# Kernel optimization log

Measured on AMD Instinct MI355X. Metric: run time of the kernel, lower is better.

The kernel has to match this reference:

```python
import jax, jax.numpy as jnp
import numpy as np

N = 100000   # total nodes in batched graph
E = 320000   # total edges
B = 128      # number of graphs in batch
D_IN = 128
H = 256
OUT = 10
L = 4        # num_layers - 1 conv layers
EPS = 1e-6


def setup_inputs() -> dict:
    key = jax.random.key(0)
    ks = jax.random.split(key, 8)
    h = jax.random.normal(ks[0], (N, D_IN), dtype=jnp.float32)
    src = jax.random.randint(ks[1], (E,), 0, N)
    dst = jax.random.randint(ks[2], (E,), 0, N)
    batch_ids = jnp.sort(jax.random.randint(ks[3], (N,), 0, B))
    s = 0.05
    W_first = jax.random.normal(ks[4], (D_IN, H), dtype=jnp.float32) * s
    b_first = jnp.zeros((H,), jnp.float32)
    W_rest = jax.random.normal(ks[5], (L - 1, H, H), dtype=jnp.float32) * s
    b_rest = jnp.zeros((L - 1, H), jnp.float32)
    gamma = jnp.ones((L, H), jnp.float32)
    beta = jnp.zeros((L, H), jnp.float32)
    mean_scale = jnp.ones((L, H), jnp.float32)
    W_pred = jax.random.normal(ks[6], (H, OUT), dtype=jnp.float32) * s
    b_pred = jnp.zeros((OUT,), jnp.float32)
    return dict(h=h, src=src, dst=dst, batch_ids=batch_ids,
                W_first=W_first, b_first=b_first, W_rest=W_rest, b_rest=b_rest,
                gamma=gamma, beta=beta, mean_scale=mean_scale,
                W_pred=W_pred, b_pred=b_pred)


def _graph_conv(h, W, b, src, dst, dinv_src, dinv_dst):
    # DGL GraphConv, norm='both': D_dst^{-1/2} A D_src^{-1/2} h W + b
    x = h * dinv_src[:, None]
    m = jax.ops.segment_sum(x[src], dst, num_segments=N)
    m = m * dinv_dst[:, None]
    return m @ W + b


def _graph_norm(h, gamma, beta, ms, batch_ids, counts):
    # GraphNorm: per-graph mean (scaled by learnable mean_scale) and std
    mean = jax.ops.segment_sum(h, batch_ids, num_segments=B) / counts[:, None]
    sub = h - mean[batch_ids] * ms
    var = jax.ops.segment_sum(sub * sub, batch_ids, num_segments=B) / counts[:, None]
    inv_std = jax.lax.rsqrt(var + EPS)
    return gamma * sub * inv_std[batch_ids] + beta


def reference(h, src, dst, batch_ids, W_first, b_first, W_rest, b_rest,
              gamma, beta, mean_scale, W_pred, b_pred):
    ones_e = jnp.ones((E,), h.dtype)
    deg_out = jnp.maximum(jax.ops.segment_sum(ones_e, src, num_segments=N), 1.0)
    deg_in = jnp.maximum(jax.ops.segment_sum(ones_e, dst, num_segments=N), 1.0)
    dinv_src = jax.lax.rsqrt(deg_out)
    dinv_dst = jax.lax.rsqrt(deg_in)
    counts = jnp.maximum(
        jax.ops.segment_sum(jnp.ones((N,), h.dtype), batch_ids, num_segments=B), 1.0)

    for i in range(L):
        x = h
        if i == 0:
            h = _graph_conv(h, W_first, b_first, src, dst, dinv_src, dinv_dst)
        else:
            h = _graph_conv(h, W_rest[i - 1], b_rest[i - 1], src, dst, dinv_src, dinv_dst)
        h = _graph_norm(h, gamma[i], beta[i], mean_scale[i], batch_ids, counts)
        if i != 0:
            h = jax.nn.relu(h) + x
        else:
            h = jax.nn.relu(h)

    pooled = jax.ops.segment_sum(h, batch_ids, num_segments=B)  # [B, H]
    # dropout is identity at eval
    return pooled @ W_pred + b_pred
```

## Files before the change

kernel.cpp:

```cpp
#include <hip/hip_runtime.h>

#define N_NODES 100000
#define N_PAD   100096
#define N_EDGES 320000
#define NB      128
#define DIN     128
#define H       256
#define OUT_DIM 10
#define EPSV    1e-6f
#define SCAN_B  256
#define PSLICES 32

typedef unsigned short bf16_t;
typedef __attribute__((ext_vector_type(8))) short bf16x8;
typedef __attribute__((ext_vector_type(4))) float f32x4;

__device__ __forceinline__ float bf2f(bf16_t u) {
    union { unsigned int i; float f; } x;
    x.i = ((unsigned int)u) << 16;
    return x.f;
}
__device__ __forceinline__ bf16_t f2bf(float f) {
    union { float f; unsigned int i; } x;
    x.f = f;
    unsigned int r = x.i + 0x7fffu + ((x.i >> 16) & 1u);
    return (bf16_t)(r >> 16);
}

__global__ void k_edge_deg(const int* __restrict__ src, const int* __restrict__ dst,
                           int* deg_out, int* deg_in) {
    int e = blockIdx.x * blockDim.x + threadIdx.x;
    if (e < N_EDGES) {
        atomicAdd(&deg_out[src[e]], 1);
        atomicAdd(&deg_in[dst[e]], 1);
    }
}

__global__ void k_dinv(const int* __restrict__ deg_out, const int* __restrict__ deg_in,
                       float* dinv_src, float* dinv_dst) {
    int n = blockIdx.x * blockDim.x + threadIdx.x;
    if (n < N_NODES) {
        dinv_src[n] = rsqrtf((float)max(deg_out[n], 1));
        dinv_dst[n] = rsqrtf((float)max(deg_in[n], 1));
    }
}

__global__ void k_gstart(const int* __restrict__ bid, int* __restrict__ gstart,
                         float* __restrict__ countsf) {
    int b = threadIdx.x;
    if (b <= NB) {
        int lo = 0, hi = N_NODES;
        while (lo < hi) {
            int mid = (lo + hi) >> 1;
            if (bid[mid] < b) lo = mid + 1; else hi = mid;
        }
        gstart[b] = lo;
    }
    __syncthreads();
    if (b < NB) countsf[b] = (float)max(gstart[b + 1] - gstart[b], 1);
}

__global__ void k_scan1(const int* __restrict__ deg, int* incl, int* bsums) {
    __shared__ int s[SCAN_B];
    int i = blockIdx.x * SCAN_B + threadIdx.x;
    int v = (i < N_NODES) ? deg[i] : 0;
    s[threadIdx.x] = v;
    __syncthreads();
    for (int d = 1; d < SCAN_B; d <<= 1) {
        int t = (threadIdx.x >= d) ? s[threadIdx.x - d] : 0;
        __syncthreads();
        s[threadIdx.x] += t;
        __syncthreads();
    }
    if (i < N_NODES) incl[i] = s[threadIdx.x];
    if (threadIdx.x == SCAN_B - 1) bsums[blockIdx.x] = s[threadIdx.x];
}

__global__ void k_scan2(const int* __restrict__ bsums, int* boffs, int nb) {
    __shared__ int s[512];
    int t = threadIdx.x;
    int v = (t < nb) ? bsums[t] : 0;
    s[t] = v;
    __syncthreads();
    for (int d = 1; d < 512; d <<= 1) {
        int x = (t >= d) ? s[t - d] : 0;
        __syncthreads();
        s[t] += x;
        __syncthreads();
    }
    if (t < nb) boffs[t] = s[t] - v;
}

__global__ void k_scan3(const int* __restrict__ deg, const int* __restrict__ incl,
                        const int* __restrict__ boffs, int* row_start, int* cursor) {
    int i = blockIdx.x * blockDim.x + threadIdx.x;
    if (i < N_NODES) {
        int ex = incl[i] - deg[i] + boffs[i / SCAN_B];
        row_start[i] = ex;
        cursor[i]    = ex;
    }
    if (i == 0) row_start[N_NODES] = N_EDGES;
}

__global__ void k_scatter(const int* __restrict__ src, const int* __restrict__ dst,
                          int* cursor, int* csr_src) {
    int e = blockIdx.x * blockDim.x + threadIdx.x;
    if (e < N_EDGES) {
        int slot = atomicAdd(&cursor[dst[e]], 1);
        csr_src[slot] = src[e];
    }
}

__global__ void k_wt_first(const float* __restrict__ W, bf16_t* __restrict__ Wt) {
    int idx = blockIdx.x * 256 + threadIdx.x;
    if (idx >= H * DIN) return;
    int c = idx / DIN, k = idx % DIN;
    Wt[idx] = f2bf(W[k * H + c]);
}
__global__ void k_wt_rest(const float* __restrict__ W, bf16_t* __restrict__ Wt) {
    int idx = blockIdx.x * 256 + threadIdx.x;
    if (idx >= 3 * H * H) return;
    int l = idx / (H * H);
    int rem = idx % (H * H);
    int c = rem / H, k = rem % H;
    Wt[idx] = f2bf(W[(size_t)l * H * H + k * H + c]);
}

__global__ void k_prescale(const float* __restrict__ h, const float* __restrict__ dinv_s,
                           bf16_t* __restrict__ hs) {
    int idx = blockIdx.x * blockDim.x + threadIdx.x;
    if (idx >= N_NODES * (DIN / 4)) return;
    int n = idx >> 5;
    float w = dinv_s[n];
    float4 v = reinterpret_cast<const float4*>(h)[idx];
    ushort4 o;
    o.x = f2bf(v.x * w); o.y = f2bf(v.y * w);
    o.z = f2bf(v.z * w); o.w = f2bf(v.w * w);
    reinterpret_cast<ushort4*>(hs)[idx] = o;
}

template <int NC, bool PS>
__global__ void k_agg(const bf16_t* __restrict__ hx, const float* __restrict__ dinv_s,
                      const float* __restrict__ dinv_d, const int* __restrict__ row_start,
                      const int* __restrict__ csr_src, bf16_t* __restrict__ m) {
    constexpr int VEC = NC / 64;
    int gid  = blockIdx.x * blockDim.x + threadIdx.x;
    int v    = gid >> 6;
    int lane = gid & 63;
    if (v >= N_NODES) return;
    float acc[VEC] = {};
    int s0 = row_start[v], s1 = row_start[v + 1];

    auto body = [&](int ei) {
        int si = csr_src[ei];
        float wv = 1.f;
        if constexpr (!PS) wv = dinv_s[si];
        if constexpr (VEC == 4) {
            ushort4 r = *reinterpret_cast<const ushort4*>(hx + (size_t)si * NC + lane * 4);
            acc[0] += bf2f(r.x) * wv; acc[1] += bf2f(r.y) * wv;
            acc[2] += bf2f(r.z) * wv; acc[3] += bf2f(r.w) * wv;
        } else {
            ushort2 r = *reinterpret_cast<const ushort2*>(hx + (size_t)si * NC + lane * 2);
            acc[0] += bf2f(r.x) * wv; acc[1] += bf2f(r.y) * wv;
        }
    };

    int e = s0;
    for (; e + 3 < s1; e += 4) { body(e); body(e + 1); body(e + 2); body(e + 3); }
    for (; e < s1; ++e) body(e);

    float wd = dinv_d[v];
    if constexpr (VEC == 4) {
        ushort4 o;
        o.x = f2bf(acc[0] * wd); o.y = f2bf(acc[1] * wd);
        o.z = f2bf(acc[2] * wd); o.w = f2bf(acc[3] * wd);
        *reinterpret_cast<ushort4*>(m + (size_t)v * NC + lane * 4) = o;
    } else {
        ushort2 o; o.x = f2bf(acc[0] * wd); o.y = f2bf(acc[1] * wd);
        *reinterpret_cast<ushort2*>(m + (size_t)v * NC + lane * 2) = o;
    }
}

template <int K>
__global__ __launch_bounds__(256) void k_gemm_mfma(const bf16_t* __restrict__ A,
                                                   const bf16_t* __restrict__ Wt,
                                                   const float* __restrict__ bias,
                                                   const int* __restrict__ bid,
                                                   bf16_t* __restrict__ C,
                                                   float* __restrict__ gsum,
                                                   float* __restrict__ gsumsq) {
    __shared__ bf16_t cT[64][H + 8];
    __shared__ int bid_lds[64];

    const int tid  = threadIdx.x;
    const int wave = tid >> 6;
    const int lane = tid & 63;
    const int row0 = blockIdx.x * 64;
    const int col0 = wave * 64;
    const int lr = lane & 15;
    const int lg = lane >> 4;

    if (tid < 64) {
        int r = row0 + tid;
        bid_lds[tid] = (r < N_NODES) ? bid[r] : -1;
    }

    const bf16_t* Ar = A  + (size_t)(row0 + lr) * K + lg * 8;
    const bf16_t* Br = Wt + (size_t)(col0 + lr) * K + lg * 8;

    f32x4 acc[4][4] = {};

    #pragma unroll
    for (int ks = 0; ks < K / 32; ++ks) {
        bf16x8 a[4], b[4];
        #pragma unroll
        for (int mt = 0; mt < 4; ++mt)
            a[mt] = *reinterpret_cast<const bf16x8*>(Ar + (size_t)mt * 16 * K + ks * 32);
        #pragma unroll
        for (int nt = 0; nt < 4; ++nt)
            b[nt] = *reinterpret_cast<const bf16x8*>(Br + (size_t)nt * 16 * K + ks * 32);
        #pragma unroll
        for (int mt = 0; mt < 4; ++mt)
            #pragma unroll
            for (int nt = 0; nt < 4; ++nt)
                acc[mt][nt] = __builtin_amdgcn_mfma_f32_16x16x32_bf16(a[mt], b[nt], acc[mt][nt], 0, 0, 0);
    }

    #pragma unroll
    for (int nt = 0; nt < 4; ++nt) {
        int c = col0 + nt * 16 + lr;
        float bs = bias[c];
        #pragma unroll
        for (int mt = 0; mt < 4; ++mt) {
            #pragma unroll
            for (int j = 0; j < 4; ++j)
                cT[mt * 16 + lg * 4 + j][c] = f2bf(acc[mt][nt][j] + bs);
        }
    }
    __syncthreads();

    #pragma unroll
    for (int it = 0; it < 8; ++it) {
        int i = it * 256 + tid;
        int r = i >> 5;
        int s = i & 31;
        *reinterpret_cast<uint4*>(C + (size_t)(row0 + r) * H + s * 8) =
            *reinterpret_cast<const uint4*>(&cT[r][s * 8]);
    }

    {
        const int c = tid;
        float s = 0.f, q = 0.f;
        int gprev = bid_lds[0];
        #pragma unroll 8
        for (int r = 0; r < 64; ++r) {
            int g = bid_lds[r];
            if (g < 0) break;
            if (g != gprev) {
                atomicAdd(&gsum[gprev * H + c], s);
                atomicAdd(&gsumsq[gprev * H + c], q);
                s = 0.f; q = 0.f; gprev = g;
            }
            float v = bf2f(cT[r][c]);
            s += v; q += v * v;
        }
        if (gprev >= 0) {
            atomicAdd(&gsum[gprev * H + c], s);
            atomicAdd(&gsumsq[gprev * H + c], q);
        }
    }
}

template <bool RES>
__global__ void k_norm(const bf16_t* __restrict__ y, const bf16_t* __restrict__ resid,
                       const int* __restrict__ bid, const float* __restrict__ gsum,
                       const float* __restrict__ gsumsq, const float* __restrict__ countsf,
                       const float* __restrict__ gamma, const float* __restrict__ beta,
                       const float* __restrict__ msc, bf16_t* __restrict__ outp) {
    int idx = blockIdx.x * blockDim.x + threadIdx.x;
    if (idx >= N_NODES * (H / 4)) return;
    int n  = idx >> 6;
    int f4 = idx & 63;
    int b  = bid[n];
    float rc = 1.0f / countsf[b];
    float4 s4  = reinterpret_cast<const float4*>(gsum)[b * 64 + f4];
    float4 q4  = reinterpret_cast<const float4*>(gsumsq)[b * 64 + f4];
    float4 g4  = reinterpret_cast<const float4*>(gamma)[f4];
    float4 be4 = reinterpret_cast<const float4*>(beta)[f4];
    float4 m4  = reinterpret_cast<const float4*>(msc)[f4];
    ushort4 yv = reinterpret_cast<const ushort4*>(y)[idx];

    auto nrm = [&](float s, float q, float ga, float be, float m, float yy) {
        float mean = s * rc, ex2 = q * rc;
        float mm   = mean * m;
        float var  = ex2 - 2.f * mean * mm + mm * mm;
        float a    = ga * rsqrtf(var + EPSV);
        return fmaxf(yy * a + (be - a * mm), 0.f);
    };
    float o0 = nrm(s4.x, q4.x, g4.x, be4.x, m4.x, bf2f(yv.x));
    float o1 = nrm(s4.y, q4.y, g4.y, be4.y, m4.y, bf2f(yv.y));
    float o2 = nrm(s4.z, q4.z, g4.z, be4.z, m4.z, bf2f(yv.z));
    float o3 = nrm(s4.w, q4.w, g4.w, be4.w, m4.w, bf2f(yv.w));
    if constexpr (RES) {
        ushort4 r = reinterpret_cast<const ushort4*>(resid)[idx];
        o0 += bf2f(r.x); o1 += bf2f(r.y); o2 += bf2f(r.z); o3 += bf2f(r.w);
    }
    ushort4 o;
    o.x = f2bf(o0); o.y = f2bf(o1); o.z = f2bf(o2); o.w = f2bf(o3);
    reinterpret_cast<ushort4*>(outp)[idx] = o;
}

__global__ void k_pool(const bf16_t* __restrict__ hf, const int* __restrict__ gstart,
                       float* pooled) {
    int b = blockIdx.x, sl = blockIdx.y, f = threadIdx.x;
    int n0 = gstart[b], n1 = gstart[b + 1];
    int cnt = n1 - n0;
    int lo = n0 + (int)((long long)cnt * sl / PSLICES);
    int hi = n0 + (int)((long long)cnt * (sl + 1) / PSLICES);
    if (lo >= hi) return;
    float s = 0.f;
    for (int n = lo; n < hi; ++n) s += bf2f(hf[(size_t)n * H + f]);
    atomicAdd(&pooled[b * H + f], s);
}

__global__ void k_pred(const float* __restrict__ pooled, const float* __restrict__ Wp,
                       const float* __restrict__ bp, float* __restrict__ outp) {
    __shared__ float row[H];
    int b = blockIdx.x;
    row[threadIdx.x] = pooled[b * H + threadIdx.x];
    __syncthreads();
    if (threadIdx.x < OUT_DIM) {
        float acc = bp[threadIdx.x];
        for (int f = 0; f < H; ++f) acc += row[f] * Wp[f * OUT_DIM + threadIdx.x];
        outp[b * OUT_DIM + threadIdx.x] = acc;
    }
}

extern "C" void kernel_launch(void* const* d_in, const int* in_sizes, int n_in,
                              void* d_out, int out_size, void* d_ws, size_t ws_size,
                              hipStream_t stream) {
    const float* h_in  = (const float*)d_in[0];
    const int*   src   = (const int*)d_in[1];
    const int*   dst   = (const int*)d_in[2];
    const int*   bid   = (const int*)d_in[3];
    const float* Wf    = (const float*)d_in[4];
    const float* bfv   = (const float*)d_in[5];
    const float* Wr    = (const float*)d_in[6];
    const float* br    = (const float*)d_in[7];
    const float* gamma = (const float*)d_in[8];
    const float* beta  = (const float*)d_in[9];
    const float* ms    = (const float*)d_in[10];
    const float* Wp    = (const float*)d_in[11];
    const float* bp    = (const float*)d_in[12];
    float* outp = (float*)d_out;

    char* w = (char*)d_ws;
    size_t off = 0;
    auto alloc = [&](size_t bytes) -> void* {
        void* p = w + off;
        off = (off + bytes + 255) & ~(size_t)255;
        return p;
    };
    bf16_t* bufA = (bf16_t*)alloc((size_t)N_PAD * H * 2);
    bf16_t* bufB = (bf16_t*)alloc((size_t)N_PAD * H * 2);
    bf16_t* bufC = (bf16_t*)alloc((size_t)N_PAD * H * 2);
    bf16_t* Wt0  = (bf16_t*)alloc((size_t)H * DIN * 2);
    bf16_t* Wt123= (bf16_t*)alloc((size_t)3 * H * H * 2);
    int* deg_out_i = (int*)alloc(N_NODES * 4);
    int* deg_in_i  = (int*)alloc(N_NODES * 4);
    float* dinv_src = (float*)alloc(N_NODES * 4);
    float* dinv_dst = (float*)alloc(N_NODES * 4);
    int* incl_tmp  = (int*)alloc(N_NODES * 4);
    int* bsums     = (int*)alloc(512 * 4);
    int* boffs     = (int*)alloc(512 * 4);
    int* row_start = (int*)alloc((N_NODES + 1) * 4);
    int* cursor    = (int*)alloc(N_NODES * 4);
    int* csr_src   = (int*)alloc(N_EDGES * 4);
    int* gstart    = (int*)alloc((NB + 1) * 4);
    float* countsf = (float*)alloc(NB * 4);
    float* gsum    = (float*)alloc((size_t)4 * NB * H * 4);
    float* gsumsq  = (float*)alloc((size_t)4 * NB * H * 4);
    float* pooled  = (float*)alloc(NB * H * 4);

    if (off > ws_size) return;

    bf16_t* hs = bufB;

    const int nscan = (N_NODES + SCAN_B - 1) / SCAN_B;

    hipMemsetAsync(deg_out_i, 0, N_NODES * 4, stream);
    hipMemsetAsync(deg_in_i, 0, N_NODES * 4, stream);
    hipMemsetAsync(gsum, 0, (size_t)4 * NB * H * 4, stream);
    hipMemsetAsync(gsumsq, 0, (size_t)4 * NB * H * 4, stream);
    hipMemsetAsync(pooled, 0, NB * H * 4, stream);

    k_edge_deg<<<(N_EDGES + 255) / 256, 256, 0, stream>>>(src, dst, deg_out_i, deg_in_i);
    k_gstart<<<1, 256, 0, stream>>>(bid, gstart, countsf);
    k_dinv<<<(N_NODES + 255) / 256, 256, 0, stream>>>(deg_out_i, deg_in_i, dinv_src, dinv_dst);
    k_scan1<<<nscan, SCAN_B, 0, stream>>>(deg_in_i, incl_tmp, bsums);
    k_scan2<<<1, 512, 0, stream>>>(bsums, boffs, nscan);
    k_scan3<<<(N_NODES + 255) / 256, 256, 0, stream>>>(deg_in_i, incl_tmp, boffs, row_start, cursor);
    k_scatter<<<(N_EDGES + 255) / 256, 256, 0, stream>>>(src, dst, cursor, csr_src);
    k_wt_first<<<(H * DIN + 255) / 256, 256, 0, stream>>>(Wf, Wt0);
    k_wt_rest<<<(3 * H * H + 255) / 256, 256, 0, stream>>>(Wr, Wt123);

    const int aggGrid  = (N_NODES + 3) / 4;
    const int normGrid = (N_NODES * (H / 4) + 255) / 256;
    const int gemmGrid = N_PAD / 64;

    k_prescale<<<(N_NODES * (DIN / 4) + 255) / 256, 256, 0, stream>>>(h_in, dinv_src, hs);
    k_agg<DIN, true><<<aggGrid, 256, 0, stream>>>(hs, nullptr, dinv_dst, row_start, csr_src, bufA);
    k_gemm_mfma<DIN><<<gemmGrid, 256, 0, stream>>>(bufA, Wt0, bfv, bid, bufB, gsum, gsumsq);
    k_norm<false><<<normGrid, 256, 0, stream>>>(bufB, nullptr, bid, gsum, gsumsq, countsf,
                                                gamma, beta, ms, bufC);

    bf16_t* hx = bufC;
    bf16_t* f1 = bufA;
    bf16_t* f2 = bufB;
    for (int i = 1; i < 4; ++i) {
        float* gs = gsum   + (size_t)i * NB * H;
        float* gq = gsumsq + (size_t)i * NB * H;
        k_agg<H, false><<<aggGrid, 256, 0, stream>>>(hx, dinv_src, dinv_dst, row_start, csr_src, f1);
        k_gemm_mfma<H><<<gemmGrid, 256, 0, stream>>>(f1, Wt123 + (size_t)(i - 1) * H * H,
                                                     br + (i - 1) * H, bid, f2, gs, gq);
        k_norm<true><<<normGrid, 256, 0, stream>>>(f2, hx, bid, gs, gq, countsf,
                                                   gamma + i * H, beta + i * H, ms + i * H, f1);
        bf16_t* nh = f1; f1 = hx; hx = nh;
    }

    k_pool<<<dim3(NB, PSLICES), H, 0, stream>>>(hx, gstart, pooled);
    k_pred<<<NB, H, 0, stream>>>(pooled, Wp, bp, outp);
}
```

Measured before the change: 636.2 us.

## Stage GEMM A tile in LDS and move GraphNorm stats to per-graph kernel

The GEMM now loads its 64-row A tile into shared memory with coalesced 16-byte loads and reads MFMA operands from LDS instead of scattered global loads, reusing the LDS buffer for the output transpose. The per-block atomic accumulation of per-graph sum and sum-of-squares is removed from the GEMM epilogue. A separate k_stats kernel instead reduces each graph's contiguous node range without atomics, which also drops the gsum memsets. The cost is an extra kernel launch per layer and a second read of the GEMM output. k_stats runs with only 128 blocks, which may underutilize the GPU.

```diff
diff --git a/kernel.cpp b/kernel.cpp
--- a/kernel.cpp
+++ b/kernel.cpp
@@ -185,12 +185,11 @@
 __global__ __launch_bounds__(256) void k_gemm_mfma(const bf16_t* __restrict__ A,
                                                    const bf16_t* __restrict__ Wt,
                                                    const float* __restrict__ bias,
-                                                   const int* __restrict__ bid,
-                                                   bf16_t* __restrict__ C,
-                                                   float* __restrict__ gsum,
-                                                   float* __restrict__ gsumsq) {
-    __shared__ bf16_t cT[64][H + 8];
-    __shared__ int bid_lds[64];
+                                                   bf16_t* __restrict__ C) {
+    __shared__ bf16_t lds_raw[64 * (H + 8)];
+    constexpr int LKA = K + 8;
+    bf16_t (*aT)[LKA] = reinterpret_cast<bf16_t (*)[LKA]>(lds_raw);
+    bf16_t (*cT)[H + 8] = reinterpret_cast<bf16_t (*)[H + 8]>(lds_raw);
 
     const int tid  = threadIdx.x;
     const int wave = tid >> 6;
@@ -200,31 +199,41 @@
     const int lr = lane & 15;
     const int lg = lane >> 4;
 
-    if (tid < 64) {
-        int r = row0 + tid;
-        bid_lds[tid] = (r < N_NODES) ? bid[r] : -1;
-    }
-
-    const bf16_t* Ar = A  + (size_t)(row0 + lr) * K + lg * 8;
-    const bf16_t* Br = Wt + (size_t)(col0 + lr) * K + lg * 8;
+    {
+        const bf16_t* Ag = A + (size_t)row0 * K;
+        constexpr int CHUNKS = 64 * K / 8;
+        #pragma unroll
+        for (int it = 0; it < CHUNKS / 256; ++it) {
+            int ci  = it * 256 + tid;
+            int row = (ci * 8) / K;
+            int col = (ci * 8) % K;
+            uint4 v = *reinterpret_cast<const uint4*>(Ag + ci * 8);
+            *reinterpret_cast<uint4*>(&aT[row][col]) = v;
+        }
+    }
+    __syncthreads();
 
     f32x4 acc[4][4] = {};
+
+    const bf16_t* Bb = Wt + (size_t)(col0 + lr) * K + lg * 8;
 
     #pragma unroll
     for (int ks = 0; ks < K / 32; ++ks) {
         bf16x8 a[4], b[4];
         #pragma unroll
         for (int mt = 0; mt < 4; ++mt)
-            a[mt] = *reinterpret_cast<const bf16x8*>(Ar + (size_t)mt * 16 * K + ks * 32);
+            a[mt] = *reinterpret_cast<const bf16x8*>(&aT[mt * 16 + lr][ks * 32 + lg * 8]);
         #pragma unroll
         for (int nt = 0; nt < 4; ++nt)
-            b[nt] = *reinterpret_cast<const bf16x8*>(Br + (size_t)nt * 16 * K + ks * 32);
+            b[nt] = *reinterpret_cast<const bf16x8*>(Bb + (size_t)nt * 16 * K + ks * 32);
         #pragma unroll
         for (int mt = 0; mt < 4; ++mt)
             #pragma unroll
             for (int nt = 0; nt < 4; ++nt)
                 acc[mt][nt] = __builtin_amdgcn_mfma_f32_16x16x32_bf16(a[mt], b[nt], acc[mt][nt], 0, 0, 0);
     }
+
+    __syncthreads();
 
     #pragma unroll
     for (int nt = 0; nt < 4; ++nt) {
@@ -247,27 +256,39 @@
         *reinterpret_cast<uint4*>(C + (size_t)(row0 + r) * H + s * 8) =
             *reinterpret_cast<const uint4*>(&cT[r][s * 8]);
     }
-
-    {
-        const int c = tid;
-        float s = 0.f, q = 0.f;
-        int gprev = bid_lds[0];
-        #pragma unroll 8
-        for (int r = 0; r < 64; ++r) {
-            int g = bid_lds[r];
-            if (g < 0) break;
-            if (g != gprev) {
-                atomicAdd(&gsum[gprev * H + c], s);
-                atomicAdd(&gsumsq[gprev * H + c], q);
-                s = 0.f; q = 0.f; gprev = g;
-            }
-            float v = bf2f(cT[r][c]);
-            s += v; q += v * v;
-        }
-        if (gprev >= 0) {
-            atomicAdd(&gsum[gprev * H + c], s);
-            atomicAdd(&gsumsq[gprev * H + c], q);
-        }
+}
+
+__global__ __launch_bounds__(512) void k_stats(const bf16_t* __restrict__ C,
+                                               const int* __restrict__ gstart,
+                                               float* __restrict__ gsum,
+                                               float* __restrict__ gsumsq) {
+    __shared__ float red[8][64][9];
+    int b   = blockIdx.x;
+    int t   = threadIdx.x;
+    int grp = t >> 6;
+    int ln  = t & 63;
+    int n0 = gstart[b], n1 = gstart[b + 1];
+    float s[4] = {}, q[4] = {};
+    for (int n = n0 + grp; n < n1; n += 8) {
+        ushort4 v = *reinterpret_cast<const ushort4*>(C + (size_t)n * H + ln * 4);
+        float x0 = bf2f(v.x), x1 = bf2f(v.y), x2 = bf2f(v.z), x3 = bf2f(v.w);
+        s[0] += x0; q[0] += x0 * x0;
+        s[1] += x1; q[1] += x1 * x1;
+        s[2] += x2; q[2] += x2 * x2;
+        s[3] += x3; q[3] += x3 * x3;
+    }
+    #pragma unroll
+    for (int j = 0; j < 4; ++j) { red[grp][ln][j] = s[j]; red[grp][ln][4 + j] = q[j]; }
+    __syncthreads();
+    if (grp == 0) {
+        #pragma unroll
+        for (int g = 1; g < 8; ++g)
+            #pragma unroll
+            for (int j = 0; j < 4; ++j) { s[j] += red[g][ln][j]; q[j] += red[g][ln][4 + j]; }
+        float4 s4 = { s[0], s[1], s[2], s[3] };
+        float4 q4 = { q[0], q[1], q[2], q[3] };
+        reinterpret_cast<float4*>(gsum   + (size_t)b * H)[ln] = s4;
+        reinterpret_cast<float4*>(gsumsq + (size_t)b * H)[ln] = q4;
     }
 }
 
@@ -378,8 +399,8 @@
     int* csr_src   = (int*)alloc(N_EDGES * 4);
     int* gstart    = (int*)alloc((NB + 1) * 4);
     float* countsf = (float*)alloc(NB * 4);
-    float* gsum    = (float*)alloc((size_t)4 * NB * H * 4);
-    float* gsumsq  = (float*)alloc((size_t)4 * NB * H * 4);
+    float* gsum    = (float*)alloc((size_t)NB * H * 4);
+    float* gsumsq  = (float*)alloc((size_t)NB * H * 4);
     float* pooled  = (float*)alloc(NB * H * 4);
 
     if (off > ws_size) return;
@@ -390,8 +411,6 @@
 
     hipMemsetAsync(deg_out_i, 0, N_NODES * 4, stream);
     hipMemsetAsync(deg_in_i, 0, N_NODES * 4, stream);
-    hipMemsetAsync(gsum, 0, (size_t)4 * NB * H * 4, stream);
-    hipMemsetAsync(gsumsq, 0, (size_t)4 * NB * H * 4, stream);
     hipMemsetAsync(pooled, 0, NB * H * 4, stream);
 
     k_edge_deg<<<(N_EDGES + 255) / 256, 256, 0, stream>>>(src, dst, deg_out_i, deg_in_i);
@@ -410,7 +429,8 @@
 
     k_prescale<<<(N_NODES * (DIN / 4) + 255) / 256, 256, 0, stream>>>(h_in, dinv_src, hs);
     k_agg<DIN, true><<<aggGrid, 256, 0, stream>>>(hs, nullptr, dinv_dst, row_start, csr_src, bufA);
-    k_gemm_mfma<DIN><<<gemmGrid, 256, 0, stream>>>(bufA, Wt0, bfv, bid, bufB, gsum, gsumsq);
+    k_gemm_mfma<DIN><<<gemmGrid, 256, 0, stream>>>(bufA, Wt0, bfv, bufB);
+    k_stats<<<NB, 512, 0, stream>>>(bufB, gstart, gsum, gsumsq);
     k_norm<false><<<normGrid, 256, 0, stream>>>(bufB, nullptr, bid, gsum, gsumsq, countsf,
                                                 gamma, beta, ms, bufC);
 
@@ -418,12 +438,11 @@
     bf16_t* f1 = bufA;
     bf16_t* f2 = bufB;
     for (int i = 1; i < 4; ++i) {
-        float* gs = gsum   + (size_t)i * NB * H;
-        float* gq = gsumsq + (size_t)i * NB * H;
         k_agg<H, false><<<aggGrid, 256, 0, stream>>>(hx, dinv_src, dinv_dst, row_start, csr_src, f1);
         k_gemm_mfma<H><<<gemmGrid, 256, 0, stream>>>(f1, Wt123 + (size_t)(i - 1) * H * H,
-                                                     br + (i - 1) * H, bid, f2, gs, gq);
-        k_norm<true><<<normGrid, 256, 0, stream>>>(f2, hx, bid, gs, gq, countsf,
+                                                     br + (i - 1) * H, f2);
+        k_stats<<<NB, 512, 0, stream>>>(f2, gstart, gsum, gsumsq);
+        k_norm<true><<<normGrid, 256, 0, stream>>>(f2, hx, bid, gsum, gsumsq, countsf,
                                                    gamma + i * H, beta + i * H, ms + i * H, f1);
         bf16_t* nh = f1; f1 = hx; hx = nh;
     }
```

New measurement: 671.1 us. 5.5% more time.
